# Performance work log

Hardware: AMD Instinct MI355X
Metric: run time of the kernel (lower is better)

Reference implementation:

```python
import jax, jax.numpy as jnp
import numpy as np

B, T, IN, H, HH, OUT = 512, 512, 6, 64, 128, 8


def setup_inputs() -> dict:
    key = jax.random.key(0)
    ks = jax.random.split(key, 14)
    def lin(k, fan_in, shape):
        s = 1.0 / np.sqrt(fan_in)
        return jax.random.uniform(k, shape, jnp.float32, -s, s)
    return {
        "x": jax.random.normal(ks[0], (B, T, IN), jnp.float32),
        # initial_linear: input_dim -> hidden
        "W_init": lin(ks[1], IN, (IN, H)), "b_init": lin(ks[2], IN, (H,)),
        # vector-field MLP: hidden -> hh -> hh -> hh -> hidden*input
        "W_in": lin(ks[3], H, (H, HH)),  "b_in": lin(ks[4], H, (HH,)),
        "W_h1": lin(ks[5], HH, (HH, HH)), "b_h1": lin(ks[6], HH, (HH,)),
        "W_h2": lin(ks[7], HH, (HH, HH)), "b_h2": lin(ks[8], HH, (HH,)),
        "W_out": lin(ks[9], HH, (HH, H * IN)), "b_out": lin(ks[10], HH, (H * IN,)),
        # final linear: hidden -> output
        "W_fin": lin(ks[11], H, (H, OUT)), "b_fin": lin(ks[12], H, (OUT,)),
    }


def reference(x, W_init, b_init, W_in, b_in, W_h1, b_h1, W_h2, b_h2,
              W_out, b_out, W_fin, b_fin):
    # vector field: f(h) -> (B, H, IN) matrix; dh/dt = f(h) @ dX/dt
    def vf(h, dX):
        z = jax.nn.relu(h @ W_in + b_in)
        z = jax.nn.relu(z @ W_h1 + b_h1)
        z = jax.nn.relu(z @ W_h2 + b_h2)
        A = jnp.tanh(z @ W_out + b_out).reshape(h.shape[0], H, IN)
        return jnp.einsum("bhi,bi->bh", A, dX)

    # h0 from initial value of the path (spline.evaluate(0) == x[:, 0])
    h0 = x[:, 0] @ W_init + b_init  # (B, H)

    # linear interpolation: dX/dt constant on each unit interval
    dX = jnp.swapaxes(x[:, 1:] - x[:, :-1], 0, 1)  # (T-1, B, IN)

    def rk4_step(h, d):
        k1 = vf(h, d)
        k2 = vf(h + 0.5 * k1, d)
        k3 = vf(h + 0.5 * k2, d)
        k4 = vf(h + k3, d)
        h_new = h + (k1 + 2.0 * k2 + 2.0 * k3 + k4) / 6.0
        return h_new, h_new

    _, hs = jax.lax.scan(rk4_step, h0, dX)  # (T-1, B, H)
    hidden = jnp.concatenate([h0[None], hs], axis=0)  # (T, B, H)
    hidden = jnp.swapaxes(hidden, 0, 1)  # (B, T, H)

    # return_sequences=True -> final linear on all steps
    return hidden @ W_fin + b_fin  # (B, T, OUT)
```

## Files before the change

### kernel.cpp

```cpp
#include <hip/hip_runtime.h>
#include <stdint.h>

namespace {

constexpr int B_   = 512;
constexpr int T_   = 512;
constexpr int IN_  = 6;
constexpr int H_   = 64;
constexpr int HH_  = 128;
constexpr int OUT_ = 8;

typedef _Float16 f16x2 __attribute__((ext_vector_type(2)));

__device__ __forceinline__ float dot2f(uint32_t w, uint32_t z, float acc) {
    return __builtin_amdgcn_fdot2(__builtin_bit_cast(f16x2, w),
                                  __builtin_bit_cast(f16x2, z), acc, false);
}

__device__ __forceinline__ uint32_t pack2f(float a, float b) {
    f16x2 p;
    p[0] = (_Float16)a;
    p[1] = (_Float16)b;
    return __builtin_bit_cast(uint32_t, p);
}

__device__ __forceinline__ float qsum4(float v) {
    int y = __builtin_amdgcn_mov_dpp(__builtin_bit_cast(int, v), 0xB1, 0xF, 0xF, true);
    v += __builtin_bit_cast(float, y);
    y = __builtin_amdgcn_mov_dpp(__builtin_bit_cast(int, v), 0x4E, 0xF, 0xF, true);
    return v + __builtin_bit_cast(float, y);
}

__device__ __forceinline__ float tanh_fast(float v) {
    float ax = fabsf(v);
    float e  = __expf(2.0f * ax);
    float r  = 1.0f - 2.0f / (e + 1.0f);
    return copysignf(r, v);
}

__global__ __launch_bounds__(512, 2) void cde_kernel(
    const float* __restrict__ x,
    const float* __restrict__ W_init, const float* __restrict__ b_init,
    const float* __restrict__ W_in,   const float* __restrict__ b_in,
    const float* __restrict__ W_h1,   const float* __restrict__ b_h1,
    const float* __restrict__ W_h2,   const float* __restrict__ b_h2,
    const float* __restrict__ W_out,  const float* __restrict__ b_out,
    const float* __restrict__ W_fin,  const float* __restrict__ b_fin,
    float* __restrict__ out)
{
    const int t  = threadIdx.x;
    const int c  = t >> 2;
    const int kq = t & 3;
    const int b0 = blockIdx.x * 2;

    __shared__ alignas(16) uint32_t hinu[2][H_ / 2];
    __shared__ alignas(16) uint32_t zAu[2][HH_ / 2];
    __shared__ alignas(16) uint32_t zBu[2][HH_ / 2];
    __shared__ float dxs[2][IN_];
    __shared__ float hbuf[2][H_];

    uint32_t w1[8], w2[16], w3[16], w4[48];
    #pragma unroll
    for (int i = 0; i < 8; ++i) {
        int k = kq * 16 + 2 * i;
        w1[i] = pack2f(W_in[k * HH_ + c], W_in[(k + 1) * HH_ + c]);
    }
    #pragma unroll
    for (int i = 0; i < 16; ++i) {
        int k = kq * 32 + 2 * i;
        w2[i] = pack2f(W_h1[k * HH_ + c], W_h1[(k + 1) * HH_ + c]);
        w3[i] = pack2f(W_h2[k * HH_ + c], W_h2[(k + 1) * HH_ + c]);
    }
    #pragma unroll
    for (int j = 0; j < 3; ++j) {
        const int col = 3 * c + j;
        #pragma unroll
        for (int i = 0; i < 16; ++i) {
            int k = kq * 32 + 2 * i;
            w4[j * 16 + i] = pack2f(W_out[k * 384 + col], W_out[(k + 1) * 384 + col]);
        }
    }
    const float bin_r = b_in[c];
    const float bh1_r = b_h1[c];
    const float bh2_r = b_h2[c];
    float bo[3];
    #pragma unroll
    for (int j = 0; j < 3; ++j) bo[j] = b_out[3 * c + j];
    const int   dbase = (c & 1) * 3;
    const int   e_own = c & 1;
    const int   r_own = c >> 1;
    const float bfin_r = (t < 128) ? b_fin[t & 7] : 0.0f;

    float wfr[8];
    #pragma unroll
    for (int j = 0; j < 8; ++j)
        wfr[j] = (t < 128) ? W_fin[((((t & 63) >> 3)) * 8 + j) * OUT_ + (t & 7)] : 0.0f;

    const size_t xb0 = (size_t)b0 * T_ * IN_;
    const size_t xb1 = (size_t)(b0 + 1) * T_ * IN_;

    const int    dde = (t < 6) ? 0 : 1;
    const int    ddi = (t < 6) ? t : t - 6;
    const size_t xbase_d = (dde == 0) ? xb0 : xb1;
    float xa = 0.f, xb = 0.f;
    if (t < 12) {
        xa = x[xbase_d + ddi];
        xb = x[xbase_d + IN_ + ddi];
        dxs[dde][ddi] = xb - xa;
        xa = xb;
        xb = x[xbase_d + 2 * IN_ + ddi];
    }

    if (t < 128) {
        int e = t >> 6, r = t & 63;
        size_t xbe = e ? xb1 : xb0;
        float s = b_init[r];
        #pragma unroll
        for (int i = 0; i < IN_; ++i) s += x[xbe + i] * W_init[i * H_ + r];
        hbuf[e][r] = s;
        ((_Float16*)hinu[e])[r] = (_Float16)s;
    }
    __syncthreads();

    float h_reg = hbuf[e_own][r_own];
    float hacc  = 0.f;

#define OUT_STAGE(TT)                                                          \
    if (t < 128) {                                                             \
        int e_ = t >> 6, o_ = t & 7, part_ = (t & 63) >> 3;                    \
        float s_ = 0.f;                                                        \
        _Pragma("unroll")                                                      \
        for (int j = 0; j < 8; ++j) s_ += hbuf[e_][part_ * 8 + j] * wfr[j];    \
        s_ += __shfl_xor(s_, 8);                                               \
        s_ += __shfl_xor(s_, 16);                                              \
        s_ += __shfl_xor(s_, 32);                                              \
        if (part_ == 0)                                                        \
            out[(size_t)(b0 + e_) * T_ * OUT_ + (size_t)(TT) * OUT_ + o_] = s_ + bfin_r; \
    }

    OUT_STAGE(0)

    float dxr[2][3];

    for (int step = 0; step < T_ - 1; ++step) {
        #pragma unroll
        for (int s4 = 0; s4 < 4; ++s4) {
            if (s4 == 0) {
                #pragma unroll
                for (int e = 0; e < 2; ++e)
                    #pragma unroll
                    for (int j = 0; j < 3; ++j) dxr[e][j] = dxs[e][dbase + j];
                if (step > 0) { OUT_STAGE(step) }
            }
            #pragma unroll
            for (int e = 0; e < 2; ++e) {
                const uint32_t* hp = hinu[e] + kq * 8;
                uint4 q0 = *reinterpret_cast<const uint4*>(hp);
                uint4 q1 = *reinterpret_cast<const uint4*>(hp + 4);
                float a = 0.f, d = 0.f;
                a = dot2f(w1[0], q0.x, a); d = dot2f(w1[1], q0.y, d);
                a = dot2f(w1[2], q0.z, a); d = dot2f(w1[3], q0.w, d);
                a = dot2f(w1[4], q1.x, a); d = dot2f(w1[5], q1.y, d);
                a = dot2f(w1[6], q1.z, a); d = dot2f(w1[7], q1.w, d);
                float z = fmaxf(bin_r + qsum4(a + d), 0.f);
                if (kq == e) ((_Float16*)zAu[e])[c] = (_Float16)z;
            }
            __syncthreads();

            #pragma unroll
            for (int e = 0; e < 2; ++e) {
                const uint32_t* zp = zAu[e] + kq * 16;
                uint4 q0 = *reinterpret_cast<const uint4*>(zp);
                uint4 q1 = *reinterpret_cast<const uint4*>(zp + 4);
                uint4 q2 = *reinterpret_cast<const uint4*>(zp + 8);
                uint4 q3 = *reinterpret_cast<const uint4*>(zp + 12);
                float a = 0.f, d = 0.f;
                #pragma unroll
                for (int m = 0; m < 4; ++m) {
                    a = dot2f(w2[m],      (&q0.x)[m], a);
                    d = dot2f(w2[4 + m],  (&q1.x)[m], d);
                    a = dot2f(w2[8 + m],  (&q2.x)[m], a);
                    d = dot2f(w2[12 + m], (&q3.x)[m], d);
                }
                float z = fmaxf(bh1_r + qsum4(a + d), 0.f);
                if (kq == e) ((_Float16*)zBu[e])[c] = (_Float16)z;
            }
            __syncthreads();

            #pragma unroll
            for (int e = 0; e < 2; ++e) {
                const uint32_t* zp = zBu[e] + kq * 16;
                uint4 q0 = *reinterpret_cast<const uint4*>(zp);
                uint4 q1 = *reinterpret_cast<const uint4*>(zp + 4);
                uint4 q2 = *reinterpret_cast<const uint4*>(zp + 8);
                uint4 q3 = *reinterpret_cast<const uint4*>(zp + 12);
                float a = 0.f, d = 0.f;
                #pragma unroll
                for (int m = 0; m < 4; ++m) {
                    a = dot2f(w3[m],      (&q0.x)[m], a);
                    d = dot2f(w3[4 + m],  (&q1.x)[m], d);
                    a = dot2f(w3[8 + m],  (&q2.x)[m], a);
                    d = dot2f(w3[12 + m], (&q3.x)[m], d);
                }
                float z = fmaxf(bh2_r + qsum4(a + d), 0.f);
                if (kq == e) ((_Float16*)zAu[e])[c] = (_Float16)z;
            }
            __syncthreads();

            float kvf[2];
            #pragma unroll
            for (int e = 0; e < 2; ++e) {
                const uint32_t* zp = zAu[e] + kq * 16;
                uint4 q0 = *reinterpret_cast<const uint4*>(zp);
                uint4 q1 = *reinterpret_cast<const uint4*>(zp + 4);
                uint4 q2 = *reinterpret_cast<const uint4*>(zp + 8);
                uint4 q3 = *reinterpret_cast<const uint4*>(zp + 12);
                float av0 = 0.f, av1 = 0.f, av2 = 0.f;
                #pragma unroll
                for (int m = 0; m < 4; ++m) {
                    uint32_t z0 = (&q0.x)[m], z1 = (&q1.x)[m], z2 = (&q2.x)[m], z3 = (&q3.x)[m];
                    av0 = dot2f(w4[m],      z0, av0); av0 = dot2f(w4[4 + m],  z1, av0);
                    av0 = dot2f(w4[8 + m],  z2, av0); av0 = dot2f(w4[12 + m], z3, av0);
                    av1 = dot2f(w4[16 + m], z0, av1); av1 = dot2f(w4[20 + m], z1, av1);
                    av1 = dot2f(w4[24 + m], z2, av1); av1 = dot2f(w4[28 + m], z3, av1);
                    av2 = dot2f(w4[32 + m], z0, av2); av2 = dot2f(w4[36 + m], z1, av2);
                    av2 = dot2f(w4[40 + m], z2, av2); av2 = dot2f(w4[44 + m], z3, av2);
                }
                av0 = qsum4(av0); av1 = qsum4(av1); av2 = qsum4(av2);
                float kvp = tanh_fast(bo[0] + av0) * dxr[e][0]
                          + tanh_fast(bo[1] + av1) * dxr[e][1]
                          + tanh_fast(bo[2] + av2) * dxr[e][2];
                kvf[e] = kvp + __shfl_xor(kvp, 4);
            }
            {
                float kv = kvf[e_own];
                hacc += ((s4 == 1 || s4 == 2) ? 2.0f : 1.0f) * kv;
                float hs;
                if (s4 < 3) {
                    hs = h_reg + ((s4 == 2) ? 1.0f : 0.5f) * kv;
                } else {
                    h_reg += hacc * (1.0f / 6.0f);
                    hacc = 0.f;
                    hs = h_reg;
                }
                if (kq == 0) {
                    ((_Float16*)hinu[e_own])[r_own] = (_Float16)hs;
                    if (s4 == 3) hbuf[e_own][r_own] = h_reg;
                }
            }
            if (s4 == 3 && step + 2 < T_ && t < 12) {
                dxs[dde][ddi] = xb - xa;
                xa = xb;
                if (step + 3 < T_) xb = x[xbase_d + (size_t)(step + 3) * IN_ + ddi];
            }
            __syncthreads();
        }
    }

    OUT_STAGE(T_ - 1)
#undef OUT_STAGE
}

}

extern "C" void kernel_launch(void* const* d_in, const int* in_sizes, int n_in,
                              void* d_out, int out_size, void* d_ws, size_t ws_size,
                              hipStream_t stream) {
    const float* x      = (const float*)d_in[0];
    const float* W_init = (const float*)d_in[1];
    const float* b_init = (const float*)d_in[2];
    const float* W_in   = (const float*)d_in[3];
    const float* b_in   = (const float*)d_in[4];
    const float* W_h1   = (const float*)d_in[5];
    const float* b_h1   = (const float*)d_in[6];
    const float* W_h2   = (const float*)d_in[7];
    const float* b_h2   = (const float*)d_in[8];
    const float* W_out  = (const float*)d_in[9];
    const float* b_out  = (const float*)d_in[10];
    const float* W_fin  = (const float*)d_in[11];
    const float* b_fin  = (const float*)d_in[12];
    float* out = (float*)d_out;

    cde_kernel<<<dim3(B_ / 2), dim3(512), 0, stream>>>(
        x, W_init, b_init, W_in, b_in, W_h1, b_h1, W_h2, b_h2,
        W_out, b_out, W_fin, b_fin, out);
}
```

Baseline: 3.930 ms.

## Process one batch element per block and double occupancy target

Each block now handles one batch row instead of two, so the grid grows from 256 to 512 blocks and launch bounds ask for 4 blocks per CU. The per-step work on each block halves, which shortens the serial chain of dot products between barriers. This trades weight reuse across two samples for more parallel blocks. Each block still reloads the full weight set into registers, and the 4-block bound squeezes the per-thread register budget, which may cause spills given the large per-thread weight arrays.

```diff
diff --git a/kernel.cpp b/kernel.cpp
--- a/kernel.cpp
+++ b/kernel.cpp
@@ -38,7 +38,7 @@
     return copysignf(r, v);
 }
 
-__global__ __launch_bounds__(512, 2) void cde_kernel(
+__global__ __launch_bounds__(512, 4) void cde_kernel(
     const float* __restrict__ x,
     const float* __restrict__ W_init, const float* __restrict__ b_init,
     const float* __restrict__ W_in,   const float* __restrict__ b_in,
@@ -51,13 +51,13 @@
     const int t  = threadIdx.x;
     const int c  = t >> 2;
     const int kq = t & 3;
-    const int b0 = blockIdx.x * 2;
-
-    __shared__ alignas(16) uint32_t hinu[2][H_ / 2];
-    __shared__ alignas(16) uint32_t zAu[2][HH_ / 2];
-    __shared__ alignas(16) uint32_t zBu[2][HH_ / 2];
-    __shared__ float dxs[2][IN_];
-    __shared__ float hbuf[2][H_];
+    const int b  = blockIdx.x;
+
+    __shared__ alignas(16) uint32_t hinu[H_ / 2];
+    __shared__ alignas(16) uint32_t zAu[HH_ / 2];
+    __shared__ alignas(16) uint32_t zBu[HH_ / 2];
+    __shared__ float dxs[IN_];
+    __shared__ float hbuf[H_];
 
     uint32_t w1[8], w2[16], w3[16], w4[48];
     #pragma unroll
@@ -86,75 +86,67 @@
     float bo[3];
     #pragma unroll
     for (int j = 0; j < 3; ++j) bo[j] = b_out[3 * c + j];
-    const int   dbase = (c & 1) * 3;
-    const int   e_own = c & 1;
-    const int   r_own = c >> 1;
-    const float bfin_r = (t < 128) ? b_fin[t & 7] : 0.0f;
+    const int  dbase = (c & 1) * 3;
+    const int  r_own = c >> 1;
+    const bool wrt   = (kq == 0) && ((c & 1) == 0);
+    const float bfin_r = (t < 64) ? b_fin[t & 7] : 0.0f;
 
     float wfr[8];
     #pragma unroll
     for (int j = 0; j < 8; ++j)
-        wfr[j] = (t < 128) ? W_fin[((((t & 63) >> 3)) * 8 + j) * OUT_ + (t & 7)] : 0.0f;
-
-    const size_t xb0 = (size_t)b0 * T_ * IN_;
-    const size_t xb1 = (size_t)(b0 + 1) * T_ * IN_;
-
-    const int    dde = (t < 6) ? 0 : 1;
-    const int    ddi = (t < 6) ? t : t - 6;
-    const size_t xbase_d = (dde == 0) ? xb0 : xb1;
+        wfr[j] = (t < 64) ? W_fin[((t >> 3) * 8 + j) * OUT_ + (t & 7)] : 0.0f;
+
+    const size_t xbase = (size_t)b * T_ * IN_;
+    const size_t obase = (size_t)b * T_ * OUT_;
+
     float xa = 0.f, xb = 0.f;
-    if (t < 12) {
-        xa = x[xbase_d + ddi];
-        xb = x[xbase_d + IN_ + ddi];
-        dxs[dde][ddi] = xb - xa;
+    if (t < IN_) {
+        xa = x[xbase + t];
+        xb = x[xbase + IN_ + t];
+        dxs[t] = xb - xa;
         xa = xb;
-        xb = x[xbase_d + 2 * IN_ + ddi];
-    }
-
-    if (t < 128) {
-        int e = t >> 6, r = t & 63;
-        size_t xbe = e ? xb1 : xb0;
-        float s = b_init[r];
+        xb = x[xbase + 2 * IN_ + t];
+    }
+
+    if (t < H_) {
+        float s = b_init[t];
         #pragma unroll
-        for (int i = 0; i < IN_; ++i) s += x[xbe + i] * W_init[i * H_ + r];
-        hbuf[e][r] = s;
-        ((_Float16*)hinu[e])[r] = (_Float16)s;
+        for (int i = 0; i < IN_; ++i) s += x[xbase + i] * W_init[i * H_ + t];
+        hbuf[t] = s;
+        ((_Float16*)hinu)[t] = (_Float16)s;
     }
     __syncthreads();
 
-    float h_reg = hbuf[e_own][r_own];
+    float h_reg = hbuf[r_own];
     float hacc  = 0.f;
 
 #define OUT_STAGE(TT)                                                          \
-    if (t < 128) {                                                             \
-        int e_ = t >> 6, o_ = t & 7, part_ = (t & 63) >> 3;                    \
+    if (t < 64) {                                                              \
+        int o_ = t & 7, part_ = t >> 3;                                        \
         float s_ = 0.f;                                                        \
         _Pragma("unroll")                                                      \
-        for (int j = 0; j < 8; ++j) s_ += hbuf[e_][part_ * 8 + j] * wfr[j];    \
+        for (int j = 0; j < 8; ++j) s_ += hbuf[part_ * 8 + j] * wfr[j];        \
         s_ += __shfl_xor(s_, 8);                                               \
         s_ += __shfl_xor(s_, 16);                                              \
         s_ += __shfl_xor(s_, 32);                                              \
         if (part_ == 0)                                                        \
-            out[(size_t)(b0 + e_) * T_ * OUT_ + (size_t)(TT) * OUT_ + o_] = s_ + bfin_r; \
+            out[obase + (size_t)(TT) * OUT_ + o_] = s_ + bfin_r;               \
     }
 
     OUT_STAGE(0)
 
-    float dxr[2][3];
+    float dxr[3];
 
     for (int step = 0; step < T_ - 1; ++step) {
         #pragma unroll
         for (int s4 = 0; s4 < 4; ++s4) {
             if (s4 == 0) {
                 #pragma unroll
-                for (int e = 0; e < 2; ++e)
-                    #pragma unroll
-                    for (int j = 0; j < 3; ++j) dxr[e][j] = dxs[e][dbase + j];
+                for (int j = 0; j < 3; ++j) dxr[j] = dxs[dbase + j];
                 if (step > 0) { OUT_STAGE(step) }
             }
-            #pragma unroll
-            for (int e = 0; e < 2; ++e) {
-                const uint32_t* hp = hinu[e] + kq * 8;
+            {
+                const uint32_t* hp = hinu + kq * 8;
                 uint4 q0 = *reinterpret_cast<const uint4*>(hp);
                 uint4 q1 = *reinterpret_cast<const uint4*>(hp + 4);
                 float a = 0.f, d = 0.f;
@@ -163,13 +155,12 @@
                 a = dot2f(w1[4], q1.x, a); d = dot2f(w1[5], q1.y, d);
                 a = dot2f(w1[6], q1.z, a); d = dot2f(w1[7], q1.w, d);
                 float z = fmaxf(bin_r + qsum4(a + d), 0.f);
-                if (kq == e) ((_Float16*)zAu[e])[c] = (_Float16)z;
-            }
-            __syncthreads();
-
-            #pragma unroll
-            for (int e = 0; e < 2; ++e) {
-                const uint32_t* zp = zAu[e] + kq * 16;
+                if (kq == 0) ((_Float16*)zAu)[c] = (_Float16)z;
+            }
+            __syncthreads();
+
+            {
+                const uint32_t* zp = zAu + kq * 16;
                 uint4 q0 = *reinterpret_cast<const uint4*>(zp);
                 uint4 q1 = *reinterpret_cast<const uint4*>(zp + 4);
                 uint4 q2 = *reinterpret_cast<const uint4*>(zp + 8);
@@ -183,13 +174,12 @@
                     d = dot2f(w2[12 + m], (&q3.x)[m], d);
                 }
                 float z = fmaxf(bh1_r + qsum4(a + d), 0.f);
-                if (kq == e) ((_Float16*)zBu[e])[c] = (_Float16)z;
-            }
-            __syncthreads();
-
-            #pragma unroll
-            for (int e = 0; e < 2; ++e) {
-                const uint32_t* zp = zBu[e] + kq * 16;
+                if (kq == 0) ((_Float16*)zBu)[c] = (_Float16)z;
+            }
+            __syncthreads();
+
+            {
+                const uint32_t* zp = zBu + kq * 16;
                 uint4 q0 = *reinterpret_cast<const uint4*>(zp);
                 uint4 q1 = *reinterpret_cast<const uint4*>(zp + 4);
                 uint4 q2 = *reinterpret_cast<const uint4*>(zp + 8);
@@ -203,14 +193,12 @@
                     d = dot2f(w3[12 + m], (&q3.x)[m], d);
                 }
                 float z = fmaxf(bh2_r + qsum4(a + d), 0.f);
-                if (kq == e) ((_Float16*)zAu[e])[c] = (_Float16)z;
-            }
-            __syncthreads();
-
-            float kvf[2];
-            #pragma unroll
-            for (int e = 0; e < 2; ++e) {
-                const uint32_t* zp = zAu[e] + kq * 16;
+                if (kq == 0) ((_Float16*)zAu)[c] = (_Float16)z;
+            }
+            __syncthreads();
+
+            {
+                const uint32_t* zp = zAu + kq * 16;
                 uint4 q0 = *reinterpret_cast<const uint4*>(zp);
                 uint4 q1 = *reinterpret_cast<const uint4*>(zp + 4);
                 uint4 q2 = *reinterpret_cast<const uint4*>(zp + 8);
@@ -227,13 +215,11 @@
                     av2 = dot2f(w4[40 + m], z2, av2); av2 = dot2f(w4[44 + m], z3, av2);
                 }
                 av0 = qsum4(av0); av1 = qsum4(av1); av2 = qsum4(av2);
-                float kvp = tanh_fast(bo[0] + av0) * dxr[e][0]
-                          + tanh_fast(bo[1] + av1) * dxr[e][1]
-                          + tanh_fast(bo[2] + av2) * dxr[e][2];
-                kvf[e] = kvp + __shfl_xor(kvp, 4);
-            }
-            {
-                float kv = kvf[e_own];
+                float kvp = tanh_fast(bo[0] + av0) * dxr[0]
+                          + tanh_fast(bo[1] + av1) * dxr[1]
+                          + tanh_fast(bo[2] + av2) * dxr[2];
+                float kv = kvp + __shfl_xor(kvp, 4);
+
                 hacc += ((s4 == 1 || s4 == 2) ? 2.0f : 1.0f) * kv;
                 float hs;
                 if (s4 < 3) {
@@ -243,15 +229,15 @@
                     hacc = 0.f;
                     hs = h_reg;
                 }
-                if (kq == 0) {
-                    ((_Float16*)hinu[e_own])[r_own] = (_Float16)hs;
-                    if (s4 == 3) hbuf[e_own][r_own] = h_reg;
-                }
-            }
-            if (s4 == 3 && step + 2 < T_ && t < 12) {
-                dxs[dde][ddi] = xb - xa;
+                if (wrt) {
+                    ((_Float16*)hinu)[r_own] = (_Float16)hs;
+                    if (s4 == 3) hbuf[r_own] = h_reg;
+                }
+            }
+            if (s4 == 3 && step + 2 < T_ && t < IN_) {
+                dxs[t] = xb - xa;
                 xa = xb;
-                if (step + 3 < T_) xb = x[xbase_d + (size_t)(step + 3) * IN_ + ddi];
+                if (step + 3 < T_) xb = x[xbase + (size_t)(step + 3) * IN_ + t];
             }
             __syncthreads();
         }
@@ -281,7 +267,7 @@
     const float* b_fin  = (const float*)d_in[12];
     float* out = (float*)d_out;
 
-    cde_kernel<<<dim3(B_ / 2), dim3(512), 0, stream>>>(
+    cde_kernel<<<dim3(B_), dim3(512), 0, stream>>>(
         x, W_init, b_init, W_in, b_in, W_h1, b_h1, W_h2, b_h2,
         W_out, b_out, W_fin, b_fin, out);
 }
```

Measured after the change: 4.024 ms. 1.02x slower.
